# Performance work log

Measured on AMD Instinct MI355X. Metric: run time of the kernel, lower is better.

Reference implementation:

```python
import jax, jax.numpy as jnp
import numpy as np

B = 64
H = 1024          # hidden_size
C = 128           # C_out
L = 2             # num_layers
T_OUT = 256


def _uniform(key, shape, scale):
    return jax.random.uniform(key, shape, jnp.float32, -scale, scale)


def setup_inputs() -> dict:
    key = jax.random.key(0)
    ks = jax.random.split(key, 12)
    s = 1.0 / np.sqrt(H)  # torch RNN init scale
    return {
        "hidden":  jax.random.normal(ks[0], (L, B, H), jnp.float32),
        "frame_0": jax.random.normal(ks[1], (B, C, 1), jnp.float32),
        # GRU layer 0 (input_size = C)
        "W_ih0": _uniform(ks[2], (3 * H, C), s),
        "W_hh0": _uniform(ks[3], (3 * H, H), s),
        "b_ih0": _uniform(ks[4], (3 * H,), s),
        "b_hh0": _uniform(ks[5], (3 * H,), s),
        # GRU layer 1 (input_size = H)
        "W_ih1": _uniform(ks[6], (3 * H, H), s),
        "W_hh1": _uniform(ks[7], (3 * H, H), s),
        "b_ih1": _uniform(ks[8], (3 * H,), s),
        "b_hh1": _uniform(ks[9], (3 * H,), s),
        # output FC: hidden_size -> C_out
        "fc_W": _uniform(ks[10], (C, H), 1.0 / np.sqrt(H)),
        "fc_b": _uniform(ks[11], (C,), 1.0 / np.sqrt(H)),
    }


def _gru_cell(x, h, W_ih, W_hh, b_ih, b_hh):
    # torch gate order: r, z, n
    gi = x @ W_ih.T + b_ih            # (B, 3H)
    gh = h @ W_hh.T + b_hh            # (B, 3H)
    i_r, i_z, i_n = jnp.split(gi, 3, axis=-1)
    h_r, h_z, h_n = jnp.split(gh, 3, axis=-1)
    r = jax.nn.sigmoid(i_r + h_r)
    z = jax.nn.sigmoid(i_z + h_z)
    n = jnp.tanh(i_n + r * h_n)
    return (1.0 - z) * n + z * h


def reference(hidden, frame_0, W_ih0, W_hh0, b_ih0, b_hh0,
              W_ih1, W_hh1, b_ih1, b_hh1, fc_W, fc_b):
    x0 = frame_0[:, :, 0]  # permute(0,2,1) then seq len 1 -> (B, C)

    def step(carry, _):
        h, x = carry                        # h: (L,B,H), x: (B,C)
        h0 = _gru_cell(x,  h[0], W_ih0, W_hh0, b_ih0, b_hh0)
        h1 = _gru_cell(h0, h[1], W_ih1, W_hh1, b_ih1, b_hh1)
        y = h1 @ fc_W.T + fc_b              # (B, C), fed back as next input
        return (jnp.stack([h0, h1]), y), y

    (_, _), ys = jax.lax.scan(step, (hidden, x0), None, length=T_OUT)
    # ys: (T, B, C) -> cat along time (dim=1 in torch) then permute -> (B, C, T)
    return jnp.transpose(ys, (1, 2, 0))
```

## Files before the change

kernel.cpp:

```cpp
#include <hip/hip_runtime.h>
#include <hip/hip_bf16.h>


typedef __bf16 bf16_t;
typedef __bf16 bf8 __attribute__((ext_vector_type(8)));
typedef float  f4  __attribute__((ext_vector_type(4)));
typedef unsigned long long u64;
typedef u64 u64x2 __attribute__((ext_vector_type(2)));

static constexpr unsigned O_FLAGS = 0;
static constexpr unsigned O_CNT   = 1024;
static constexpr unsigned O_B0F   = 4096;
static constexpr unsigned O_X0    = O_B0F + 12288;
static constexpr unsigned O_H0B   = O_X0  + 16384;
static constexpr unsigned O_H1B   = O_H0B + 131072;
static constexpr unsigned O_GH0   = O_H1B + 262144;
static constexpr unsigned O_GH1   = O_GH0 + 786432;
static constexpr unsigned O_W0F   = O_GH1 + 786432;

#define LDS_EXTRA 98304
#define LDS_SIZE  131072

__device__ __forceinline__ void sfence() { __builtin_amdgcn_sched_barrier(0); }

__device__ __forceinline__ float sigmoidf_(float x) { return 1.f / (1.f + __expf(-x)); }
__device__ __forceinline__ float tanhf_(float x) {
  float e = __expf(-2.f * fabsf(x));
  float t = (1.f - e) / (1.f + e);
  return x < 0.f ? -t : t;
}

__device__ __forceinline__ u64 llc_ld64(const void* p) {
  return __hip_atomic_load((u64*)p, __ATOMIC_RELAXED, __HIP_MEMORY_SCOPE_AGENT);
}
__device__ __forceinline__ float llc_ldf(const float* p) {
  return __hip_atomic_load((float*)p, __ATOMIC_RELAXED, __HIP_MEMORY_SCOPE_AGENT);
}
__device__ __forceinline__ void llc_stf(float* p, float v) {
  __hip_atomic_store(p, v, __ATOMIC_RELAXED, __HIP_MEMORY_SCOPE_AGENT);
}
__device__ __forceinline__ void llc_st32(unsigned* p, unsigned v) {
  __hip_atomic_store(p, v, __ATOMIC_RELAXED, __HIP_MEMORY_SCOPE_AGENT);
}


template<int NKS, int RS>
__device__ __forceinline__ void gemm3(const bf16_t* __restrict__ Afm,
                                      const char* lds, int lane, int rt,
                                      f4& c0, f4& c1, f4& c2)
{
  const int lo = lane & 15, hi = lane >> 4;
  const bf16_t* ap = Afm + (size_t)rt * (NKS * 512) + lane * 8;
  const int sw = lo & 7;
  const char* l0 = lds + lo * RS;
  const char* l1 = lds + (16 + lo) * RS;
  const char* l2 = lds + (32 + lo) * RS;
  u64 ab0[16], ab1[16];
#pragma unroll
  for (int p = 0; p < 16; ++p) {
    if (p < NKS) { ab0[p] = llc_ld64(ap + p * 512); ab1[p] = llc_ld64(ap + p * 512 + 4); }
  }
  int xo0 = (hi ^ sw) * 16;
  bf8 b0 = *(const bf8*)(l0 + xo0);
  bf8 b1 = *(const bf8*)(l1 + xo0);
  bf8 b2 = *(const bf8*)(l2 + xo0);
#pragma unroll
  for (int ks = 0; ks < NKS; ++ks) {
    bf8 nb0, nb1, nb2;
    if (ks + 1 < NKS) {
      const int nxo = (((ks + 1) * 4 + hi) ^ sw) * 16;
      nb0 = *(const bf8*)(l0 + nxo);
      nb1 = *(const bf8*)(l1 + nxo);
      nb2 = *(const bf8*)(l2 + nxo);
    }
    u64x2 tt; tt.x = ab0[ks % 16]; tt.y = ab1[ks % 16];
    bf8 a = __builtin_bit_cast(bf8, tt);
    if (ks + 16 < NKS) {
      ab0[ks % 16] = llc_ld64(ap + (ks + 16) * 512);
      ab1[ks % 16] = llc_ld64(ap + (ks + 16) * 512 + 4);
    }
    c0 = __builtin_amdgcn_mfma_f32_16x16x32_bf16(a, b0, c0, 0, 0, 0);
    c1 = __builtin_amdgcn_mfma_f32_16x16x32_bf16(a, b1, c1, 0, 0, 0);
    c2 = __builtin_amdgcn_mfma_f32_16x16x32_bf16(a, b2, c2, 0, 0, 0);
    b0 = nb0; b1 = nb1; b2 = nb2;
  }
}

__device__ __forceinline__ f4 gemm1(const bf16_t* __restrict__ Afm,
                                    const char* lds, int lane, int rt)
{
  const int lo = lane & 15, hi = lane >> 4;
  const bf16_t* ap = Afm + (size_t)rt * 16384 + lane * 8;
  const int sw = lo & 7;
  const char* lb = lds + lo * 2048;
  f4 acc = {0.f, 0.f, 0.f, 0.f};
  u64 ab0[16], ab1[16];
#pragma unroll
  for (int p = 0; p < 16; ++p) {
    ab0[p] = llc_ld64(ap + p * 512); ab1[p] = llc_ld64(ap + p * 512 + 4);
  }
  bf8 b = *(const bf8*)(lb + (hi ^ sw) * 16);
#pragma unroll
  for (int ks = 0; ks < 32; ++ks) {
    bf8 nb;
    if (ks + 1 < 32) nb = *(const bf8*)(lb + ((((ks + 1) * 4 + hi) ^ sw) * 16));
    u64x2 tt; tt.x = ab0[ks % 16]; tt.y = ab1[ks % 16];
    bf8 a = __builtin_bit_cast(bf8, tt);
    if (ks + 16 < 32) {
      ab0[ks % 16] = llc_ld64(ap + (ks + 16) * 512);
      ab1[ks % 16] = llc_ld64(ap + (ks + 16) * 512 + 4);
    }
    acc = __builtin_amdgcn_mfma_f32_16x16x32_bf16(a, b, acc, 0, 0, 0);
    b = nb;
  }
  return acc;
}

__device__ __forceinline__ void gh_store(f4 c0, f4 c1, f4 c2, float* __restrict__ dst,
                                         float br, float bz, float bn, int wv, int hi, int col)
{
#pragma unroll
  for (int q = 0; q < 4; ++q) {
    int row = wv * 16 + hi * 4 + q;
    size_t gb = (size_t)row * 3072 + col;
    llc_stf(dst + gb,        c0[q] + br);
    llc_stf(dst + gb + 1024, c1[q] + bz);
    llc_stf(dst + gb + 2048, c2[q] + bn);
  }
}

__device__ __forceinline__ void gh_prefetch(const float* __restrict__ ghw,
                                            int wv, int hi, int col,
                                            f4& g0, f4& g1, f4& g2)
{
#pragma unroll
  for (int q = 0; q < 4; ++q) {
    size_t gb = (size_t)(wv * 16 + hi * 4 + q) * 3072 + col;
    g0[q] = llc_ldf(ghw + gb);
    g1[q] = llc_ldf(ghw + gb + 1024);
    g2[q] = llc_ldf(ghw + gb + 2048);
  }
}

__device__ __forceinline__ void gru_apply(f4 c0, f4 c1, f4 c2, f4 g0, f4 g1, f4 g2,
                                          float br, float bz, float bn,
                                          float hreg[4], bf16_t* __restrict__ hb,
                                          int hoff, int lo)
{
#pragma unroll
  for (int q = 0; q < 4; ++q) {
    float r = sigmoidf_(c0[q] + br + g0[q]);
    float z = sigmoidf_(c1[q] + bz + g1[q]);
    float n = tanhf_  (c2[q] + bn + r * g2[q]);
    float hv = (1.f - z) * n + z * hreg[q];
    hreg[q] = hv;
    unsigned my = (unsigned)__builtin_bit_cast(unsigned short, (bf16_t)hv);
    unsigned ot = __shfl_xor(my, 1, 64);
    if ((lo & 1) == 0)
      llc_st32((unsigned*)(hb + hoff + q * 8), my | (ot << 16));
  }
}

__global__ void __launch_bounds__(256, 1)
rnn_persist(const float* __restrict__ hidden, const float* __restrict__ frame0,
            const float* __restrict__ Wih0, const float* __restrict__ Whh0,
            const float* __restrict__ bih0, const float* __restrict__ bhh0,
            const float* __restrict__ Wih1, const float* __restrict__ Whh1,
            const float* __restrict__ bih1, const float* __restrict__ bhh1,
            const float* __restrict__ fcW, const float* __restrict__ fcb,
            float* __restrict__ out, char* __restrict__ ws)
{
  extern __shared__ char smem[];
  const int tid = threadIdx.x;
  const int bid = blockIdx.x;
  const int gid = bid >> 6;
  const int lid = bid & 63;
  const int lane = tid & 63;
  const int wv = tid >> 6;
  const int lo = lane & 15, hi = lane >> 4;

  unsigned* flags = (unsigned*)(ws + O_FLAGS);
  unsigned* cntA0 = (unsigned*)(ws + O_CNT);
  unsigned* cntA3 = (unsigned*)(ws + O_CNT + 256);
  unsigned* cntB1 = (unsigned*)(ws + O_CNT + 512);
  unsigned* cntB2 = (unsigned*)(ws + O_CNT + 768);
  float*  b0f  = (float*)(ws + O_B0F);
  bf16_t* x0b  = (bf16_t*)(ws + O_X0);
  bf16_t* h0b  = (bf16_t*)(ws + O_H0B);
  bf16_t* h1b  = (bf16_t*)(ws + O_H1B);
  float*  gh0w = (float*)(ws + O_GH0);
  float*  gh1w = (float*)(ws + O_GH1);
  bf16_t* w0fb = (bf16_t*)(ws + O_W0F);

  auto signal_cnt = [&](unsigned* cnt) {
    sfence();
    asm volatile("s_waitcnt vmcnt(0)" ::: "memory");
    __syncthreads();
    if (tid == 0)
      (void)__hip_atomic_fetch_add(cnt, 1u, __ATOMIC_RELAXED, __HIP_MEMORY_SCOPE_AGENT);
  };
  auto wait_cnt = [&](unsigned* cnt, unsigned target) {
    if (tid == 0) {
      while (__hip_atomic_load(cnt, __ATOMIC_RELAXED, __HIP_MEMORY_SCOPE_AGENT) < target) {}
    }
    __syncthreads();
    sfence();
  };
  auto barrier_heavy = [&]() {
    __syncthreads();
    if (tid == 0)
      __hip_atomic_store(&flags[bid], 1u, __ATOMIC_RELEASE, __HIP_MEMORY_SCOPE_AGENT);
    if (tid < 64) {
      const u64* fp = (const u64*)(flags) + tid * 2;
      for (;;) {
        u64 a = llc_ld64(fp), b = llc_ld64(fp + 1);
        if ((unsigned)a && (unsigned)(a >> 32) && (unsigned)b && (unsigned)(b >> 32)) break;
        __builtin_amdgcn_s_sleep(1);
      }
    }
    __syncthreads();
    __builtin_amdgcn_fence(__ATOMIC_ACQUIRE, "agent");
    sfence();
  };

  const int col = lid * 16 + lo;
  const int hoff = (wv * 32 + (lid >> 1)) * 512
                 + ((((lid & 1) << 1) + (lo >> 3)) * 16 + hi * 4) * 8 + (lo & 7);
  float hreg[4];

  {
#pragma unroll
    for (int it = 0; it < 2; ++it) {
      int idx = bid * 512 + it * 256 + tid;
      float v = hidden[idx];
      int layer = idx >> 16, rc = idx & 65535;
      int row = rc >> 10, c = rc & 1023;
      int f = ((row >> 4) * 32 + (c >> 5)) * 512 + (((c >> 3) & 3) * 16 + (row & 15)) * 8 + (c & 7);
      if (layer == 0) h0b[f] = (bf16_t)v;
      else            h1b[65536 + f] = (bf16_t)v;
    }
    if (gid == 0 || gid == 2) {
#pragma unroll
      for (int q = 0; q < 4; ++q) {
        int row = wv * 16 + hi * 4 + q;
        hreg[q] = hidden[(gid == 0 ? 0 : 65536) + (size_t)row * 1024 + col];
      }
    }
    if (bid < 32) {
      int idx = bid * 256 + tid;
      int row = idx >> 7, c = idx & 127;
      int f = ((row >> 4) * 4 + (c >> 5)) * 512 + (((c >> 3) & 3) * 16 + (row & 15)) * 8 + (c & 7);
      x0b[f] = (bf16_t)frame0[idx];
    }

    float* wih  = (float*)smem;
    float* fcbl = wih + 1536;
    float* fcwt = fcbl + 128;
    const int jbase = bid * 12;
    for (int i = 0; i < 6; ++i) { int ii = tid + 256 * i; wih[ii] = Wih0[(size_t)jbase * 128 + ii]; }
    if (tid < 128) fcbl[tid] = fcb[tid];
    __syncthreads();
    if (tid < 12) {
      float s = bih0[jbase + tid];
      for (int c = 0; c < 128; ++c) s += wih[tid * 128 + c] * fcbl[c];
      b0f[jbase + tid] = s;
    }
    for (int kt = 0; kt < 16; ++kt) {
      __syncthreads();
      for (int i = 0; i < 32; ++i) {
        int ii = tid + 256 * i; int c = ii >> 6, x = ii & 63;
        fcwt[ii] = fcW[(size_t)c * 1024 + kt * 64 + x];
      }
      __syncthreads();
      int x = tid & 63, jg = tid >> 6;
      for (int jj = 0; jj < 3; ++jj) {
        int j = jg * 3 + jj;
        float s = 0.f;
#pragma unroll 16
        for (int c = 0; c < 128; ++c) s += wih[j * 128 + c] * fcwt[c * 64 + x];
        w0fb[(size_t)(jbase + j) * 1024 + kt * 64 + x] = (bf16_t)s;
      }
    }
  }
  barrier_heavy();

  float brM = 0.f, bzM = 0.f, bnM = 0.f, br0 = 0.f, bz0 = 0.f, bn0 = 0.f, fcbr = 0.f;
  if (gid == 0) {
    brM = b0f[col]; bzM = b0f[1024 + col]; bnM = b0f[2048 + col];
    br0 = bih0[col]; bz0 = bih0[1024 + col]; bn0 = bih0[2048 + col];
  } else if (gid == 1) {
    brM = bhh0[col]; bzM = bhh0[1024 + col]; bnM = bhh0[2048 + col];
    if (lid < 8) fcbr = fcb[col];
  } else if (gid == 2) {
    brM = bih1[col]; bzM = bih1[1024 + col]; bnM = bih1[2048 + col];
  } else {
    brM = bhh1[col]; bzM = bhh1[1024 + col]; bnM = bhh1[2048 + col];
  }

  {
    if (gid == 0) {
      for (int i = 0; i < 24; ++i) {
        int cc = tid + 256 * i;
        int w = cc >> 7, x = cc & 127;
        int g = w >> 4, r = w & 15;
        size_t grow = (size_t)g * 1024 + lid * 16 + r;
        bf8 v = *(const bf8*)(w0fb + grow * 1024 + x * 8);
        *(bf8*)(smem + w * 2048 + ((x ^ (w & 7)) * 16)) = v;
      }
      for (int i = 0; i < 3; ++i) {
        int cc = tid + 256 * i;
        int w = cc >> 4, x = cc & 15;
        int g = w >> 4, r = w & 15;
        size_t grow = (size_t)g * 1024 + lid * 16 + r;
        const float* src = Wih0 + grow * 128 + x * 8;
        bf8 v;
#pragma unroll
        for (int e = 0; e < 8; ++e) v[e] = (bf16_t)src[e];
        *(bf8*)(smem + LDS_EXTRA + w * 256 + ((x ^ (w & 7)) * 16)) = v;
      }
    } else {
      const float* Wsrc = (gid == 1) ? Whh0 : (gid == 2) ? Wih1 : Whh1;
      for (int i = 0; i < 24; ++i) {
        int cc = tid + 256 * i;
        int w = cc >> 7, x = cc & 127;
        int g = w >> 4, r = w & 15;
        size_t grow = (size_t)g * 1024 + lid * 16 + r;
        const float* src = Wsrc + grow * 1024 + x * 8;
        bf8 v;
#pragma unroll
        for (int e = 0; e < 8; ++e) v[e] = (bf16_t)src[e];
        *(bf8*)(smem + w * 2048 + ((x ^ (w & 7)) * 16)) = v;
      }
      if (gid == 1 && lid < 8) {
        for (int i = 0; i < 8; ++i) {
          int cc = tid + 256 * i;
          int w = cc >> 7, x = cc & 127;
          const float* src = fcW + (size_t)(lid * 16 + w) * 1024 + x * 8;
          bf8 v;
#pragma unroll
          for (int e = 0; e < 8; ++e) v[e] = (bf16_t)src[e];
          *(bf8*)(smem + LDS_EXTRA + w * 2048 + ((x ^ (w & 7)) * 16)) = v;
        }
      }
    }
    if (gid == 1) {
      __syncthreads();
      f4 c0 = {0.f,0.f,0.f,0.f}, c1 = {0.f,0.f,0.f,0.f}, c2 = {0.f,0.f,0.f,0.f};
      gemm3<32, 2048>(h0b, (const char*)smem, lane, wv, c0, c1, c2);
      gh_store(c0, c1, c2, gh0w, brM, bzM, bnM, wv, hi, col);
      signal_cnt(cntB1);
    }
  }

  for (int t = 0; t < 256; ++t) {
    const unsigned tgt = 64u * (t + 1);
    const bf16_t* h1prev = h1b + ((t + 1) & 1) * 65536;

    if (gid == 0) {
      wait_cnt(cntB1, tgt);
      if (t > 0) wait_cnt(cntB2, tgt - 64);
      f4 g0, g1, g2;
      gh_prefetch(gh0w, wv, hi, col, g0, g1, g2);
      f4 c0 = {0.f,0.f,0.f,0.f}, c1 = {0.f,0.f,0.f,0.f}, c2 = {0.f,0.f,0.f,0.f};
      if (t == 0) {
        gemm3<4, 256>(x0b, (const char*)smem + LDS_EXTRA, lane, wv, c0, c1, c2);
        gru_apply(c0, c1, c2, g0, g1, g2, br0, bz0, bn0, hreg, h0b, hoff, lo);
      } else {
        gemm3<32, 2048>(h1prev, (const char*)smem, lane, wv, c0, c1, c2);
        gru_apply(c0, c1, c2, g0, g1, g2, brM, bzM, bnM, hreg, h0b, hoff, lo);
      }
      signal_cnt(cntA0);
    } else if (gid == 3) {
      if (t > 0) wait_cnt(cntB2, tgt - 64);
      f4 c0 = {0.f,0.f,0.f,0.f}, c1 = {0.f,0.f,0.f,0.f}, c2 = {0.f,0.f,0.f,0.f};
      gemm3<32, 2048>(h1prev, (const char*)smem, lane, wv, c0, c1, c2);
      gh_store(c0, c1, c2, gh1w, brM, bzM, bnM, wv, hi, col);
      signal_cnt(cntA3);
    } else if (gid == 1) {
      if (lid < 8 && t > 0) {
        wait_cnt(cntB2, tgt - 64);
        f4 y = gemm1(h1prev, (const char*)smem + LDS_EXTRA, lane, wv);
#pragma unroll
        for (int q = 0; q < 4; ++q) {
          int row = wv * 16 + hi * 4 + q;
          out[(size_t)row * 32768 + (size_t)col * 256 + (t - 1)] = y[q] + fcbr;
        }
      }
      wait_cnt(cntA0, tgt);
      if (t < 255) {
        f4 c0 = {0.f,0.f,0.f,0.f}, c1 = {0.f,0.f,0.f,0.f}, c2 = {0.f,0.f,0.f,0.f};
        gemm3<32, 2048>(h0b, (const char*)smem, lane, wv, c0, c1, c2);
        gh_store(c0, c1, c2, gh0w, brM, bzM, bnM, wv, hi, col);
      }
      signal_cnt(cntB1);
    } else {
      wait_cnt(cntA0, tgt);
      wait_cnt(cntA3, tgt);
      f4 g0, g1, g2;
      gh_prefetch(gh1w, wv, hi, col, g0, g1, g2);
      f4 c0 = {0.f,0.f,0.f,0.f}, c1 = {0.f,0.f,0.f,0.f}, c2 = {0.f,0.f,0.f,0.f};
      gemm3<32, 2048>(h0b, (const char*)smem, lane, wv, c0, c1, c2);
      gru_apply(c0, c1, c2, g0, g1, g2, brM, bzM, bnM, hreg,
                h1b + (t & 1) * 65536, hoff, lo);
      signal_cnt(cntB2);
    }
  }

  if (gid == 1 && lid < 8) {
    wait_cnt(cntB2, 64u * 256);
    const bf16_t* h1last = h1b + 65536;
    f4 y = gemm1(h1last, (const char*)smem + LDS_EXTRA, lane, wv);
#pragma unroll
    for (int q = 0; q < 4; ++q) {
      int row = wv * 16 + hi * 4 + q;
      out[(size_t)row * 32768 + (size_t)col * 256 + 255] = y[q] + fcbr;
    }
  }
}

extern "C" void kernel_launch(void* const* d_in, const int* in_sizes, int n_in,
                              void* d_out, int out_size, void* d_ws, size_t ws_size,
                              hipStream_t stream)
{
  const float* hidden = (const float*)d_in[0];
  const float* frame0 = (const float*)d_in[1];
  const float* Wih0 = (const float*)d_in[2];
  const float* Whh0 = (const float*)d_in[3];
  const float* bih0 = (const float*)d_in[4];
  const float* bhh0 = (const float*)d_in[5];
  const float* Wih1 = (const float*)d_in[6];
  const float* Whh1 = (const float*)d_in[7];
  const float* bih1 = (const float*)d_in[8];
  const float* bhh1 = (const float*)d_in[9];
  const float* fcW  = (const float*)d_in[10];
  const float* fcb  = (const float*)d_in[11];
  float* out = (float*)d_out;
  char*  ws  = (char*)d_ws;

  hipMemsetAsync(ws, 0, 4096, stream);

  hipFuncSetAttribute((const void*)rnn_persist,
                      hipFuncAttributeMaxDynamicSharedMemorySize, LDS_SIZE);

  void* args[] = { (void*)&hidden, (void*)&frame0, (void*)&Wih0, (void*)&Whh0,
                   (void*)&bih0, (void*)&bhh0, (void*)&Wih1, (void*)&Whh1,
                   (void*)&bih1, (void*)&bhh1, (void*)&fcW, (void*)&fcb,
                   (void*)&out, (void*)&ws };
  hipError_t err = hipLaunchCooperativeKernel((const void*)rnn_persist,
                                              dim3(256), dim3(256), args, LDS_SIZE, stream);
  if (err != hipSuccess) {
    rnn_persist<<<dim3(256), dim3(256), LDS_SIZE, stream>>>(
        hidden, frame0, Wih0, Whh0, bih0, bhh0, Wih1, Whh1, bih1, bhh1, fcW, fcb, out, ws);
  }
}
```

Before: 4.150 ms.

## Replace atomic counters with per-block flags, column-major gh buffers, full A prefetch

```diff
diff --git a/kernel.cpp b/kernel.cpp
--- a/kernel.cpp
+++ b/kernel.cpp
@@ -5,11 +5,12 @@
 typedef __bf16 bf16_t;
 typedef __bf16 bf8 __attribute__((ext_vector_type(8)));
 typedef float  f4  __attribute__((ext_vector_type(4)));
+typedef float  f2  __attribute__((ext_vector_type(2)));
 typedef unsigned long long u64;
 typedef u64 u64x2 __attribute__((ext_vector_type(2)));
 
 static constexpr unsigned O_FLAGS = 0;
-static constexpr unsigned O_CNT   = 1024;
+static constexpr unsigned O_FLG   = 1024;
 static constexpr unsigned O_B0F   = 4096;
 static constexpr unsigned O_X0    = O_B0F + 12288;
 static constexpr unsigned O_H0B   = O_X0  + 16384;
@@ -33,14 +34,18 @@
 __device__ __forceinline__ u64 llc_ld64(const void* p) {
   return __hip_atomic_load((u64*)p, __ATOMIC_RELAXED, __HIP_MEMORY_SCOPE_AGENT);
 }
-__device__ __forceinline__ float llc_ldf(const float* p) {
-  return __hip_atomic_load((float*)p, __ATOMIC_RELAXED, __HIP_MEMORY_SCOPE_AGENT);
-}
-__device__ __forceinline__ void llc_stf(float* p, float v) {
-  __hip_atomic_store(p, v, __ATOMIC_RELAXED, __HIP_MEMORY_SCOPE_AGENT);
+__device__ __forceinline__ unsigned llc_ld32(const unsigned* p) {
+  return __hip_atomic_load((unsigned*)p, __ATOMIC_RELAXED, __HIP_MEMORY_SCOPE_AGENT);
 }
 __device__ __forceinline__ void llc_st32(unsigned* p, unsigned v) {
   __hip_atomic_store(p, v, __ATOMIC_RELAXED, __HIP_MEMORY_SCOPE_AGENT);
+}
+__device__ __forceinline__ void llc_st2f(float* p, float x, float y) {
+  f2 v = {x, y};
+  __hip_atomic_store((u64*)p, __builtin_bit_cast(u64, v), __ATOMIC_RELAXED, __HIP_MEMORY_SCOPE_AGENT);
+}
+__device__ __forceinline__ f2 llc_ld2f(const float* p) {
+  return __builtin_bit_cast(f2, llc_ld64(p));
 }
 
 
@@ -55,10 +60,11 @@
   const char* l0 = lds + lo * RS;
   const char* l1 = lds + (16 + lo) * RS;
   const char* l2 = lds + (32 + lo) * RS;
-  u64 ab0[16], ab1[16];
-#pragma unroll
-  for (int p = 0; p < 16; ++p) {
-    if (p < NKS) { ab0[p] = llc_ld64(ap + p * 512); ab1[p] = llc_ld64(ap + p * 512 + 4); }
+  u64 a0[NKS], a1[NKS];
+#pragma unroll
+  for (int p = 0; p < NKS; ++p) {
+    a0[p] = llc_ld64(ap + p * 512);
+    a1[p] = llc_ld64(ap + p * 512 + 4);
   }
   int xo0 = (hi ^ sw) * 16;
   bf8 b0 = *(const bf8*)(l0 + xo0);
@@ -73,12 +79,8 @@
       nb1 = *(const bf8*)(l1 + nxo);
       nb2 = *(const bf8*)(l2 + nxo);
     }
-    u64x2 tt; tt.x = ab0[ks % 16]; tt.y = ab1[ks % 16];
+    u64x2 tt; tt.x = a0[ks]; tt.y = a1[ks];
     bf8 a = __builtin_bit_cast(bf8, tt);
-    if (ks + 16 < NKS) {
-      ab0[ks % 16] = llc_ld64(ap + (ks + 16) * 512);
-      ab1[ks % 16] = llc_ld64(ap + (ks + 16) * 512 + 4);
-    }
     c0 = __builtin_amdgcn_mfma_f32_16x16x32_bf16(a, b0, c0, 0, 0, 0);
     c1 = __builtin_amdgcn_mfma_f32_16x16x32_bf16(a, b1, c1, 0, 0, 0);
     c2 = __builtin_amdgcn_mfma_f32_16x16x32_bf16(a, b2, c2, 0, 0, 0);
@@ -94,52 +96,44 @@
   const int sw = lo & 7;
   const char* lb = lds + lo * 2048;
   f4 acc = {0.f, 0.f, 0.f, 0.f};
-  u64 ab0[16], ab1[16];
-#pragma unroll
-  for (int p = 0; p < 16; ++p) {
-    ab0[p] = llc_ld64(ap + p * 512); ab1[p] = llc_ld64(ap + p * 512 + 4);
+  u64 a0[32], a1[32];
+#pragma unroll
+  for (int p = 0; p < 32; ++p) {
+    a0[p] = llc_ld64(ap + p * 512);
+    a1[p] = llc_ld64(ap + p * 512 + 4);
   }
   bf8 b = *(const bf8*)(lb + (hi ^ sw) * 16);
 #pragma unroll
   for (int ks = 0; ks < 32; ++ks) {
     bf8 nb;
     if (ks + 1 < 32) nb = *(const bf8*)(lb + ((((ks + 1) * 4 + hi) ^ sw) * 16));
-    u64x2 tt; tt.x = ab0[ks % 16]; tt.y = ab1[ks % 16];
+    u64x2 tt; tt.x = a0[ks]; tt.y = a1[ks];
     bf8 a = __builtin_bit_cast(bf8, tt);
-    if (ks + 16 < 32) {
-      ab0[ks % 16] = llc_ld64(ap + (ks + 16) * 512);
-      ab1[ks % 16] = llc_ld64(ap + (ks + 16) * 512 + 4);
-    }
     acc = __builtin_amdgcn_mfma_f32_16x16x32_bf16(a, b, acc, 0, 0, 0);
     b = nb;
   }
   return acc;
 }
 
-__device__ __forceinline__ void gh_store(f4 c0, f4 c1, f4 c2, float* __restrict__ dst,
-                                         float br, float bz, float bn, int wv, int hi, int col)
-{
-#pragma unroll
-  for (int q = 0; q < 4; ++q) {
-    int row = wv * 16 + hi * 4 + q;
-    size_t gb = (size_t)row * 3072 + col;
-    llc_stf(dst + gb,        c0[q] + br);
-    llc_stf(dst + gb + 1024, c1[q] + bz);
-    llc_stf(dst + gb + 2048, c2[q] + bn);
-  }
-}
-
-__device__ __forceinline__ void gh_prefetch(const float* __restrict__ ghw,
-                                            int wv, int hi, int col,
-                                            f4& g0, f4& g1, f4& g2)
-{
-#pragma unroll
-  for (int q = 0; q < 4; ++q) {
-    size_t gb = (size_t)(wv * 16 + hi * 4 + q) * 3072 + col;
-    g0[q] = llc_ldf(ghw + gb);
-    g1[q] = llc_ldf(ghw + gb + 1024);
-    g2[q] = llc_ldf(ghw + gb + 2048);
-  }
+__device__ __forceinline__ void gh_store_cm(f4 c0, f4 c1, f4 c2, float* __restrict__ dst,
+                                            float br, float bz, float bn, int base)
+{
+  llc_st2f(dst + base,              c0[0] + br, c0[1] + br);
+  llc_st2f(dst + base + 2,          c0[2] + br, c0[3] + br);
+  llc_st2f(dst + 65536 + base,      c1[0] + bz, c1[1] + bz);
+  llc_st2f(dst + 65536 + base + 2,  c1[2] + bz, c1[3] + bz);
+  llc_st2f(dst + 131072 + base,     c2[0] + bn, c2[1] + bn);
+  llc_st2f(dst + 131072 + base + 2, c2[2] + bn, c2[3] + bn);
+}
+__device__ __forceinline__ void gh_load_cm(const float* __restrict__ src, int base,
+                                           f4& g0, f4& g1, f4& g2)
+{
+  f2 a = llc_ld2f(src + base),              b = llc_ld2f(src + base + 2);
+  f2 c = llc_ld2f(src + 65536 + base),      d = llc_ld2f(src + 65536 + base + 2);
+  f2 e = llc_ld2f(src + 131072 + base),     f = llc_ld2f(src + 131072 + base + 2);
+  g0[0] = a[0]; g0[1] = a[1]; g0[2] = b[0]; g0[3] = b[1];
+  g1[0] = c[0]; g1[1] = c[1]; g1[2] = d[0]; g1[3] = d[1];
+  g2[0] = e[0]; g2[1] = e[1]; g2[2] = f[0]; g2[3] = f[1];
 }
 
 __device__ __forceinline__ void gru_apply(f4 c0, f4 c1, f4 c2, f4 g0, f4 g1, f4 g2,
@@ -180,10 +174,10 @@
   const int lo = lane & 15, hi = lane >> 4;
 
   unsigned* flags = (unsigned*)(ws + O_FLAGS);
-  unsigned* cntA0 = (unsigned*)(ws + O_CNT);
-  unsigned* cntA3 = (unsigned*)(ws + O_CNT + 256);
-  unsigned* cntB1 = (unsigned*)(ws + O_CNT + 512);
-  unsigned* cntB2 = (unsigned*)(ws + O_CNT + 768);
+  unsigned* flgA0 = (unsigned*)(ws + O_FLG);
+  unsigned* flgA3 = (unsigned*)(ws + O_FLG + 256);
+  unsigned* flgB1 = (unsigned*)(ws + O_FLG + 512);
+  unsigned* flgB2 = (unsigned*)(ws + O_FLG + 768);
   float*  b0f  = (float*)(ws + O_B0F);
   bf16_t* x0b  = (bf16_t*)(ws + O_X0);
   bf16_t* h0b  = (bf16_t*)(ws + O_H0B);
@@ -192,16 +186,24 @@
   float*  gh1w = (float*)(ws + O_GH1);
   bf16_t* w0fb = (bf16_t*)(ws + O_W0F);
 
-  auto signal_cnt = [&](unsigned* cnt) {
+  auto signal_flag = [&](unsigned* arr, unsigned val) {
     sfence();
     asm volatile("s_waitcnt vmcnt(0)" ::: "memory");
     __syncthreads();
-    if (tid == 0)
-      (void)__hip_atomic_fetch_add(cnt, 1u, __ATOMIC_RELAXED, __HIP_MEMORY_SCOPE_AGENT);
+    if (tid == 0) llc_st32(&arr[lid], val);
   };
-  auto wait_cnt = [&](unsigned* cnt, unsigned target) {
-    if (tid == 0) {
-      while (__hip_atomic_load(cnt, __ATOMIC_RELAXED, __HIP_MEMORY_SCOPE_AGENT) < target) {}
+  auto wait1 = [&](unsigned* arr, unsigned g) {
+    if (tid < 64) { while (!__all(llc_ld32(&arr[tid]) >= g)) {} }
+    __syncthreads();
+    sfence();
+  };
+  auto wait2 = [&](unsigned* a, unsigned ga, unsigned* b, unsigned gb) {
+    if (tid < 64) {
+      for (;;) {
+        unsigned va = llc_ld32(&a[tid]);
+        unsigned vb = llc_ld32(&b[tid]);
+        if (__all(va >= ga && vb >= gb)) break;
+      }
     }
     __syncthreads();
     sfence();
@@ -226,6 +228,7 @@
   const int col = lid * 16 + lo;
   const int hoff = (wv * 32 + (lid >> 1)) * 512
                  + ((((lid & 1) << 1) + (lo >> 3)) * 16 + hi * 4) * 8 + (lo & 7);
+  const int ghbase = col * 64 + wv * 16 + hi * 4;
   float hreg[4];
 
   {
@@ -347,20 +350,19 @@
       __syncthreads();
       f4 c0 = {0.f,0.f,0.f,0.f}, c1 = {0.f,0.f,0.f,0.f}, c2 = {0.f,0.f,0.f,0.f};
       gemm3<32, 2048>(h0b, (const char*)smem, lane, wv, c0, c1, c2);
-      gh_store(c0, c1, c2, gh0w, brM, bzM, bnM, wv, hi, col);
-      signal_cnt(cntB1);
+      gh_store_cm(c0, c1, c2, gh0w, brM, bzM, bnM, ghbase);
+      signal_flag(flgB1, 1);
     }
   }
 
   for (int t = 0; t < 256; ++t) {
-    const unsigned tgt = 64u * (t + 1);
     const bf16_t* h1prev = h1b + ((t + 1) & 1) * 65536;
 
     if (gid == 0) {
-      wait_cnt(cntB1, tgt);
-      if (t > 0) wait_cnt(cntB2, tgt - 64);
+      if (t == 0) wait1(flgB1, 1);
+      else        wait2(flgB1, (unsigned)(t + 1), flgB2, (unsigned)t);
       f4 g0, g1, g2;
-      gh_prefetch(gh0w, wv, hi, col, g0, g1, g2);
+      gh_load_cm(gh0w, ghbase, g0, g1, g2);
       f4 c0 = {0.f,0.f,0.f,0.f}, c1 = {0.f,0.f,0.f,0.f}, c2 = {0.f,0.f,0.f,0.f};
       if (t == 0) {
         gemm3<4, 256>(x0b, (const char*)smem + LDS_EXTRA, lane, wv, c0, c1, c2);
@@ -369,16 +371,16 @@
         gemm3<32, 2048>(h1prev, (const char*)smem, lane, wv, c0, c1, c2);
         gru_apply(c0, c1, c2, g0, g1, g2, brM, bzM, bnM, hreg, h0b, hoff, lo);
       }
-      signal_cnt(cntA0);
+      signal_flag(flgA0, (unsigned)(t + 1));
     } else if (gid == 3) {
-      if (t > 0) wait_cnt(cntB2, tgt - 64);
+      if (t > 0) wait1(flgB2, (unsigned)t);
       f4 c0 = {0.f,0.f,0.f,0.f}, c1 = {0.f,0.f,0.f,0.f}, c2 = {0.f,0.f,0.f,0.f};
       gemm3<32, 2048>(h1prev, (const char*)smem, lane, wv, c0, c1, c2);
-      gh_store(c0, c1, c2, gh1w, brM, bzM, bnM, wv, hi, col);
-      signal_cnt(cntA3);
+      gh_store_cm(c0, c1, c2, gh1w, brM, bzM, bnM, ghbase);
+      signal_flag(flgA3, (unsigned)(t + 1));
     } else if (gid == 1) {
       if (lid < 8 && t > 0) {
-        wait_cnt(cntB2, tgt - 64);
+        wait1(flgB2, (unsigned)t);
         f4 y = gemm1(h1prev, (const char*)smem + LDS_EXTRA, lane, wv);
 #pragma unroll
         for (int q = 0; q < 4; ++q) {
@@ -386,28 +388,27 @@
           out[(size_t)row * 32768 + (size_t)col * 256 + (t - 1)] = y[q] + fcbr;
         }
       }
-      wait_cnt(cntA0, tgt);
+      wait1(flgA0, (unsigned)(t + 1));
       if (t < 255) {
         f4 c0 = {0.f,0.f,0.f,0.f}, c1 = {0.f,0.f,0.f,0.f}, c2 = {0.f,0.f,0.f,0.f};
         gemm3<32, 2048>(h0b, (const char*)smem, lane, wv, c0, c1, c2);
-        gh_store(c0, c1, c2, gh0w, brM, bzM, bnM, wv, hi, col);
-      }
-      signal_cnt(cntB1);
+        gh_store_cm(c0, c1, c2, gh0w, brM, bzM, bnM, ghbase);
+      }
+      signal_flag(flgB1, (unsigned)(t + 2));
     } else {
-      wait_cnt(cntA0, tgt);
-      wait_cnt(cntA3, tgt);
+      wait2(flgA0, (unsigned)(t + 1), flgA3, (unsigned)(t + 1));
       f4 g0, g1, g2;
-      gh_prefetch(gh1w, wv, hi, col, g0, g1, g2);
+      gh_load_cm(gh1w, ghbase, g0, g1, g2);
       f4 c0 = {0.f,0.f,0.f,0.f}, c1 = {0.f,0.f,0.f,0.f}, c2 = {0.f,0.f,0.f,0.f};
       gemm3<32, 2048>(h0b, (const char*)smem, lane, wv, c0, c1, c2);
       gru_apply(c0, c1, c2, g0, g1, g2, brM, bzM, bnM, hreg,
                 h1b + (t & 1) * 65536, hoff, lo);
-      signal_cnt(cntB2);
+      signal_flag(flgB2, (unsigned)(t + 1));
     }
   }
 
   if (gid == 1 && lid < 8) {
-    wait_cnt(cntB2, 64u * 256);
+    wait1(flgB2, 256u);
     const bf16_t* h1last = h1b + 65536;
     f4 y = gemm1(h1last, (const char*)smem + LDS_EXTRA, lane, wv);
 #pragma unroll
```

Result: slower. 4.551 ms (+9.7%).
